# Kernel optimization log

Hardware: AMD Instinct MI355X
Metric: run time of the kernel (lower is better)

The kernel has to match this reference:

```python
import jax, jax.numpy as jnp
import numpy as np

P = 16            # num_patches = 224 // 14
T = P * P         # patches per image (256)
K = 5             # top-k templates
SIM_THR = 0.05
PATCH_THR = 2.0


def _idx2loc(idx):
    # flat patch index -> (w, h) float location, matching convert_index2location
    return jnp.stack([(idx % P).astype(jnp.float32), (idx // P).astype(jnp.float32)], axis=-1)


def setup_inputs() -> dict:
    key = jax.random.key(0)
    k1, k2, k3, k4 = jax.random.split(key, 4)
    B, N, C = 8, 32, 768
    src_feats = jax.random.normal(k1, (B, N, C, P, P), dtype=jnp.float32)
    tar_feat = jax.random.normal(k2, (B, C, P, P), dtype=jnp.float32)
    src_masks = (jax.random.uniform(k3, (B, N, P, P)) > 0.3).astype(jnp.float32)
    tar_mask = (jax.random.uniform(k4, (B, P, P)) > 0.3).astype(jnp.float32)
    return {"src_feats": src_feats, "tar_feat": tar_feat,
            "src_masks": src_masks, "tar_mask": tar_mask}


def reference(src_feats, tar_feat, src_masks, tar_mask):
    B, N, C = src_feats.shape[:3]
    # masks are already at feature resolution -> interpolate is identity; flatten
    tarm = tar_mask.reshape(B, T)                                   # (B, T)
    srcm = src_masks.reshape(B, N, T)                               # (B, N, T)
    # L2-normalize features over channel dim (F.normalize)
    tf = tar_feat / jnp.clip(jnp.linalg.norm(tar_feat, axis=1, keepdims=True), 1e-12)
    tf = tf.reshape(B, C, T)                                        # (B, C, T)
    sf = src_feats / jnp.clip(jnp.linalg.norm(src_feats, axis=2, keepdims=True), 1e-12)
    sf = sf.reshape(B, N, C, T)                                     # (B, N, C, S)
    # dense cosine similarity, masked, then thresholded to 0
    sim = jnp.einsum('bct,bncs->bnts', tf, sf)                      # (B, N, T, S)
    sim = sim * srcm[:, :, None, :] * tarm[:, None, :, None]
    sim = jnp.where(sim < SIM_THR, 0.0, sim)
    # dual nearest-neighbor search ('tar2src' direction)
    score_t2s = sim.max(axis=3)                                     # (B, N, T)
    idx_t2s = sim.argmax(axis=3).astype(jnp.int32)
    score_s2t = sim.max(axis=2)                                     # (B, N, S)
    idx_s2t = sim.argmax(axis=2).astype(jnp.int32)
    mask_sim = score_t2s >= SIM_THR
    # cycle consistency: tar -> src -> tar
    idx_s2s = jnp.take_along_axis(idx_s2t, idx_t2s, axis=2)         # (B, N, T)
    dist = jnp.linalg.norm(_idx2loc(idx_s2s) - _idx2loc(jnp.arange(T))[None, None], axis=-1)
    sim_s2s = jnp.take_along_axis(score_s2t, idx_t2s, axis=2)
    mask_cycle = (dist <= PATCH_THR) & (sim_s2s >= SIM_THR)
    # non-zero / in-mask filtering
    mask_t2s = jnp.take_along_axis(srcm, idx_t2s, axis=2)           # (B, N, T)
    mask_nz = tarm[:, None, :] * mask_t2s * (idx_s2t != 0) * (idx_t2s != 0)
    mask_all = (mask_sim & mask_cycle) * mask_nz                    # (B, N, T) float
    match_counts = mask_all.sum(axis=2)                             # (B, N)
    sim_avg = jnp.where(match_counts > 0,
                        (score_t2s * mask_all).sum(axis=2) / float(T), 0.0)
    # top-k template selection
    score_src, id_src = jax.lax.top_k(sim_avg, K)                   # (B, K)
    sel = lambda a: jnp.take_along_axis(a, id_src[:, :, None], axis=1)
    pred_mask = sel(mask_all)                                       # (B, K, T)
    score_pts = sel(score_t2s)                                      # (B, K, T)
    src_loc = _idx2loc(sel(idx_t2s)).astype(jnp.int32)              # (B, K, T, 2)
    # format_prediction: -1 outside mask, (w, h) coords inside
    grid = _idx2loc(jnp.arange(T)).astype(jnp.int32)                # (T, 2)
    nz = (pred_mask != 0)[..., None]
    tar_pts = jnp.where(nz, grid[None, None], -1)                   # (B, K, T, 2)
    src_pts = jnp.where(nz, src_loc, -1)                            # (B, K, T, 2)
    return id_src, score_src, score_pts, tar_pts, src_pts, match_counts
```

## Files before the change

kernel.cpp:

```cpp
#include <hip/hip_runtime.h>

#define T_PATCH 256
#define C_DIM   768
#define NCH     48
#define N_B     8
#define N_N     32

typedef unsigned short u16;
typedef u16   u16x8  __attribute__((ext_vector_type(8)));
typedef u16   u16x4  __attribute__((ext_vector_type(4)));
typedef short s16x8  __attribute__((ext_vector_type(8)));
typedef float f32x16 __attribute__((ext_vector_type(16)));

__device__ __forceinline__ unsigned rne16(unsigned u) {
    return (u + 0x7fffu + ((u >> 16) & 1u)) >> 16;
}

__device__ __forceinline__ void split3(float x, u16& o0, u16& o1, u16& o2) {
    unsigned u0 = rne16(__float_as_uint(x));
    float f0 = __uint_as_float(u0 << 16);
    float r1 = x - f0;
    unsigned u1 = rne16(__float_as_uint(r1));
    float f1 = __uint_as_float(u1 << 16);
    float r2 = r1 - f1;
    o0 = (u16)u0; o1 = (u16)u1; o2 = (u16)(__float_as_uint(r2) >> 16);
}

__device__ __forceinline__ void gll16(const u16* g, u16* l) {
    __builtin_amdgcn_global_load_lds(
        (const __attribute__((address_space(1))) unsigned int*)g,
        (__attribute__((address_space(3))) unsigned int*)l, 16, 0, 0);
}

__global__ void tar_split_kernel(const float* __restrict__ tar,
                                 u16* __restrict__ tS0, u16* __restrict__ tS1,
                                 u16* __restrict__ tS2, float* __restrict__ partT) {
    int blk = blockIdx.x;
    int b = blk / NCH, c = blk - b * NCH;
    int tid = threadIdx.x;
    int g = tid >> 8, t = tid & 255;
    const float* tb = tar + (size_t)b * C_DIM * T_PATCH;
    float ss = 0.f;
    u16x8 v0, v1, v2;
    #pragma unroll
    for (int j = 0; j < 8; ++j) {
        float x = tb[(c * 16 + g * 8 + j) * T_PATCH + t];
        u16 a, bb, cc;
        split3(x, a, bb, cc);
        v0[j] = a; v1[j] = bb; v2[j] = cc;
        ss = fmaf(x, x, ss);
    }
    size_t off = ((size_t)blk * 512 + tid) * 8;
    *(u16x8*)(tS0 + off) = v0;
    *(u16x8*)(tS1 + off) = v1;
    *(u16x8*)(tS2 + off) = v2;
    __shared__ float sq[512];
    sq[tid] = ss;
    __syncthreads();
    if (tid < 256) partT[blk * 256 + tid] = sq[tid] + sq[tid + 256];
}

__global__ void invt_kernel(const float* __restrict__ partT,
                            const float* __restrict__ tar_mask,
                            float* __restrict__ w_invT) {
    int b = blockIdx.x, t = threadIdx.x;
    float s = 0.f;
    for (int c = 0; c < NCH; ++c) s += partT[(b * NCH + c) * 256 + t];
    float tm = tar_mask[b * 256 + t];
    w_invT[b * 256 + t] = (tm != 0.f) ? 1.f / fmaxf(sqrtf(s), 1e-12f) : 0.f;
}

__launch_bounds__(512, 4)
__global__ void sim_kernel(const float* __restrict__ src_feats,
                           const u16* __restrict__ tS0, const u16* __restrict__ tS1,
                           const u16* __restrict__ tS2,
                           const float* __restrict__ w_invT,
                           const float* __restrict__ src_masks,
                           float* __restrict__ w_rowv, int* __restrict__ w_rowi,
                           float* __restrict__ w_s2tv, int* __restrict__ w_s2ti) {
    __shared__ __align__(16) u16 SM[36864];
    u16* Af0 = SM;
    u16* Af1 = SM + 8192;
    u16* Af2 = SM + 16384;
    u16* Bf0 = SM + 24576;
    u16* Bf1 = SM + 28672;
    u16* Bf2 = SM + 32768;
    float* sqv  = (float*)(SM);
    float* rowv = (float*)(SM + 1024);
    int*   rowi = (int*)  (SM + 3072);
    float* colv = (float*)(SM + 5120);
    int*   coli = (int*)  (SM + 6144);
    float* invT = (float*)(SM + 7168);
    float* invS = (float*)(SM + 7680);

    int bh = blockIdx.x;
    int b    = bh & 7;
    int loc  = bh >> 3;
    int n    = loc >> 1;
    int half = loc & 1;
    int bn   = b * N_N + n;
    int lbh  = bn * 2 + half;

    int tid = threadIdx.x;
    int lane = tid & 63, w = tid >> 6;
    int wm = w >> 1, wn = w & 1;
    int h = lane >> 5, l5 = lane & 31;
    int colB = tid & 127, qB = tid >> 7;
    int gq = qB >> 1, quad = qB & 1;

    const float* psrc = src_feats + (size_t)bn * C_DIM * T_PATCH
                      + (size_t)(gq * 8 + quad * 4) * T_PATCH + half * 128 + colB;
    size_t abase = (size_t)b * NCH * 4096 + (size_t)tid * 8;
    const u16* pga0 = tS0 + abase;
    const u16* pga1 = tS1 + abase;
    const u16* pga2 = tS2 + abase;

    f32x16 acc[2][2];
    #pragma unroll
    for (int i = 0; i < 2; ++i)
        #pragma unroll
        for (int j = 0; j < 2; ++j) acc[i][j] = (f32x16)0.0f;

    float sss = 0.f;

    {
        float yv[4];
        #pragma unroll
        for (int j = 0; j < 4; ++j) yv[j] = psrc[j * T_PATCH];
        psrc += 4096;
        gll16(pga0, Af0 + tid * 8);
        gll16(pga1, Af1 + tid * 8);
        gll16(pga2, Af2 + tid * 8);
        pga0 += 4096; pga1 += 4096; pga2 += 4096;
        u16x4 b0v, b1v, b2v;
        #pragma unroll
        for (int j = 0; j < 4; ++j) {
            u16 a, bb, cc;
            split3(yv[j], a, bb, cc);
            b0v[j] = a; b1v[j] = bb; b2v[j] = cc;
            sss = fmaf(yv[j], yv[j], sss);
        }
        int bslot = (gq * 128 + colB) * 8 + quad * 4;
        *(u16x4*)(Bf0 + bslot) = b0v;
        *(u16x4*)(Bf1 + bslot) = b1v;
        *(u16x4*)(Bf2 + bslot) = b2v;
    }
    __syncthreads();

    for (int c = 0; c < NCH; ++c) {
        int p = c & 1;
        bool pf = (c < NCH - 1);

        float yv[4];
        if (pf) {
            #pragma unroll
            for (int j = 0; j < 4; ++j) yv[j] = psrc[j * T_PATCH];
            psrc += 4096;
        }
        if (pf) {
            int adst = (p ^ 1) * 4096 + tid * 8;
            gll16(pga0, Af0 + adst);
            gll16(pga1, Af1 + adst);
            gll16(pga2, Af2 + adst);
            pga0 += 4096; pga1 += 4096; pga2 += 4096;
        }

        __builtin_amdgcn_s_setprio(1);
        s16x8 a0[2], a1[2], a2[2];
        {
            const u16* Ab = Af0 + p * 4096 + (h * 256 + wm * 64 + l5) * 8;
            #pragma unroll
            for (int i = 0; i < 2; ++i) a0[i] = *(const s16x8*)(Ab + i * 256);
            Ab = Af1 + p * 4096 + (h * 256 + wm * 64 + l5) * 8;
            #pragma unroll
            for (int i = 0; i < 2; ++i) a1[i] = *(const s16x8*)(Ab + i * 256);
            Ab = Af2 + p * 4096 + (h * 256 + wm * 64 + l5) * 8;
            #pragma unroll
            for (int i = 0; i < 2; ++i) a2[i] = *(const s16x8*)(Ab + i * 256);
        }
        #pragma unroll
        for (int j = 0; j < 2; ++j) {
            int boff = p * 2048 + (h * 128 + wn * 64 + j * 32 + l5) * 8;
            s16x8 b0 = *(const s16x8*)(Bf0 + boff);
            s16x8 b1 = *(const s16x8*)(Bf1 + boff);
            s16x8 b2 = *(const s16x8*)(Bf2 + boff);
            #pragma unroll
            for (int i = 0; i < 2; ++i) {
                acc[i][j] = __builtin_amdgcn_mfma_f32_32x32x16_bf16(a0[i], b0, acc[i][j], 0, 0, 0);
                acc[i][j] = __builtin_amdgcn_mfma_f32_32x32x16_bf16(a0[i], b1, acc[i][j], 0, 0, 0);
                acc[i][j] = __builtin_amdgcn_mfma_f32_32x32x16_bf16(a1[i], b0, acc[i][j], 0, 0, 0);
                acc[i][j] = __builtin_amdgcn_mfma_f32_32x32x16_bf16(a1[i], b1, acc[i][j], 0, 0, 0);
                acc[i][j] = __builtin_amdgcn_mfma_f32_32x32x16_bf16(a0[i], b2, acc[i][j], 0, 0, 0);
                acc[i][j] = __builtin_amdgcn_mfma_f32_32x32x16_bf16(a2[i], b0, acc[i][j], 0, 0, 0);
            }
        }
        __builtin_amdgcn_s_setprio(0);

        if (pf) {
            u16x4 b0v, b1v, b2v;
            #pragma unroll
            for (int j = 0; j < 4; ++j) {
                u16 a, bb, cc;
                split3(yv[j], a, bb, cc);
                b0v[j] = a; b1v[j] = bb; b2v[j] = cc;
                sss = fmaf(yv[j], yv[j], sss);
            }
            int bslot = (p ^ 1) * 2048 + (gq * 128 + colB) * 8 + quad * 4;
            *(u16x4*)(Bf0 + bslot) = b0v;
            *(u16x4*)(Bf1 + bslot) = b1v;
            *(u16x4*)(Bf2 + bslot) = b2v;
        }
        __syncthreads();
    }

    sqv[tid] = sss;
    if (tid < 256) invT[tid] = w_invT[b * 256 + tid];
    __syncthreads();
    if (tid < 128) {
        float ns = sqrtf(sqv[tid] + sqv[tid + 128] + sqv[tid + 256] + sqv[tid + 384]);
        float smv = src_masks[bn * 256 + half * 128 + tid];
        invS[tid] = (smv != 0.f) ? 1.f / fmaxf(ns, 1e-12f) : 0.f;
    }
    __syncthreads();

    float isv[2]; int sgl[2];
    #pragma unroll
    for (int j = 0; j < 2; ++j) {
        isv[j] = invS[wn * 64 + j * 32 + l5];
        sgl[j] = half * 128 + wn * 64 + j * 32 + l5;
    }
    float cbv[2]; int cbi[2];
    #pragma unroll
    for (int j = 0; j < 2; ++j) { cbv[j] = -1.f; cbi[j] = 0; }

    #pragma unroll
    for (int i = 0; i < 2; ++i) {
        #pragma unroll
        for (int r = 0; r < 16; ++r) {
            int trow = wm * 64 + i * 32 + (r & 3) + 8 * (r >> 2) + 4 * h;
            float it = invT[trow];
            float v[2];
            #pragma unroll
            for (int j = 0; j < 2; ++j) {
                float x = acc[i][j][r] * it * isv[j];
                v[j] = (x >= 0.05f) ? x : 0.f;
            }
            float bv = -1.f; int bi = 0;
            #pragma unroll
            for (int j = 0; j < 2; ++j)
                if (v[j] > bv) { bv = v[j]; bi = sgl[j]; }
            #pragma unroll
            for (int off = 1; off < 32; off <<= 1) {
                float ov = __shfl_xor(bv, off, 64);
                int   oi = __shfl_xor(bi, off, 64);
                if (ov > bv || (ov == bv && oi < bi)) { bv = ov; bi = oi; }
            }
            if (l5 == 0) { rowv[wn * 256 + trow] = bv; rowi[wn * 256 + trow] = bi; }
            #pragma unroll
            for (int j = 0; j < 2; ++j)
                if (v[j] > cbv[j]) { cbv[j] = v[j]; cbi[j] = trow; }
        }
    }
    #pragma unroll
    for (int j = 0; j < 2; ++j) {
        float bv = cbv[j]; int bi = cbi[j];
        float ov = __shfl_xor(bv, 32, 64);
        int   oi = __shfl_xor(bi, 32, 64);
        if (ov > bv || (ov == bv && oi < bi)) { bv = ov; bi = oi; }
        if (h == 0) { colv[wm * 128 + wn * 64 + j * 32 + l5] = bv;
                      coli[wm * 128 + wn * 64 + j * 32 + l5] = bi; }
    }
    __syncthreads();
    if (tid < 256) {
        float v0 = rowv[tid];       int i0 = rowi[tid];
        float v1 = rowv[256 + tid]; int i1 = rowi[256 + tid];
        if (v1 > v0 || (v1 == v0 && i1 < i0)) { v0 = v1; i0 = i1; }
        w_rowv[lbh * 256 + tid] = v0;
        w_rowi[lbh * 256 + tid] = i0;
    }
    if (tid < 128) {
        float bv = colv[tid]; int bi = coli[tid];
        #pragma unroll
        for (int q = 1; q < 4; ++q) {
            float ov = colv[q * 128 + tid]; int oi = coli[q * 128 + tid];
            if (ov > bv || (ov == bv && oi < bi)) { bv = ov; bi = oi; }
        }
        w_s2tv[bn * 256 + half * 128 + tid] = bv;
        w_s2ti[bn * 256 + half * 128 + tid] = bi;
    }
}

__global__ void combine_kernel(const float* __restrict__ w_rowv, const int* __restrict__ w_rowi,
                               const float* __restrict__ w_s2tv, const int* __restrict__ w_s2ti,
                               const float* __restrict__ src_masks, const float* __restrict__ tar_mask,
                               float* __restrict__ w_score, float* __restrict__ w_mall,
                               float* __restrict__ w_savg, int* __restrict__ w_idx,
                               float* __restrict__ out) {
    int bn = blockIdx.x; int b = bn >> 5; int t = threadIdx.x;
    __shared__ float sc_s2t[256]; __shared__ int ix_s2t[256];
    __shared__ float sm[256];
    __shared__ float red[8];
    sc_s2t[t] = w_s2tv[bn * 256 + t];
    ix_s2t[t] = w_s2ti[bn * 256 + t];
    sm[t]     = src_masks[bn * 256 + t];
    float v0 = w_rowv[(bn * 2) * 256 + t];     int i0 = w_rowi[(bn * 2) * 256 + t];
    float v1 = w_rowv[(bn * 2 + 1) * 256 + t]; int i1 = w_rowi[(bn * 2 + 1) * 256 + t];
    float st2s; int i;
    if (v1 > v0 || (v1 == v0 && i1 < i0)) { st2s = v1; i = i1; }
    else                                  { st2s = v0; i = i0; }
    float tmv = tar_mask[b * 256 + t];
    __syncthreads();

    bool msim = st2s >= 0.05f;
    int is2s = ix_s2t[i];
    int dw = (is2s & 15) - (t & 15);
    int dh = (is2s >> 4) - (t >> 4);
    bool cyc = (dw * dw + dh * dh <= 4) && (sc_s2t[i] >= 0.05f);
    float mnz = tmv * sm[i] *
                ((ix_s2t[t] != 0) ? 1.f : 0.f) *
                ((i != 0) ? 1.f : 0.f);
    float mall = (msim && cyc) ? mnz : 0.f;
    w_score[bn * 256 + t] = st2s;
    w_mall[bn * 256 + t]  = mall;
    w_idx[bn * 256 + t]   = i;

    float cnt = mall, svs = st2s * mall;
    #pragma unroll
    for (int off = 1; off < 64; off <<= 1) {
        cnt += __shfl_xor(cnt, off, 64);
        svs += __shfl_xor(svs, off, 64);
    }
    if ((t & 63) == 0) {
        red[(t >> 6) * 2]     = cnt;
        red[(t >> 6) * 2 + 1] = svs;
    }
    __syncthreads();
    if (t == 0) {
        float c = red[0] + red[2] + red[4] + red[6];
        float s = red[1] + red[3] + red[5] + red[7];
        w_savg[bn] = (c > 0.f) ? (s * (1.f / 256.f)) : 0.f;
        out[51280 + bn] = c;
    }
}

__global__ void final_kernel(const float* __restrict__ w_score,
                             const float* __restrict__ w_mall,
                             const float* __restrict__ w_savg,
                             const int*   __restrict__ w_idx,
                             float* __restrict__ out) {
    int b = blockIdx.x, tid = threadIdx.x;
    __shared__ float savg[32];
    __shared__ int   topid[5];
    __shared__ float topv[5];
    if (tid < 32) savg[tid] = w_savg[b * 32 + tid];
    __syncthreads();
    if (tid == 0) {
        unsigned used = 0;
        for (int k = 0; k < 5; ++k) {
            float bv = -1e30f; int bi = 0;
            for (int n = 0; n < 32; ++n) {
                if (!((used >> n) & 1u) && savg[n] > bv) { bv = savg[n]; bi = n; }
            }
            used |= (1u << bi);
            topid[k] = bi; topv[k] = bv;
        }
    }
    __syncthreads();
    if (tid < 5) {
        out[b * 5 + tid]      = (float)topid[tid];
        out[40 + b * 5 + tid] = topv[tid];
    }
    int t = tid;
    for (int k = 0; k < 5; ++k) {
        int bn = b * 32 + topid[k];
        float sc = w_score[bn * 256 + t];
        float ma = w_mall[bn * 256 + t];
        int   ii = w_idx[bn * 256 + t];
        int o = (b * 5 + k) * 256 + t;
        out[80 + o] = sc;
        bool nz = (ma != 0.f);
        out[10320 + 2 * o]     = nz ? (float)(t & 15)  : -1.f;
        out[10320 + 2 * o + 1] = nz ? (float)(t >> 4)  : -1.f;
        out[30800 + 2 * o]     = nz ? (float)(ii & 15) : -1.f;
        out[30800 + 2 * o + 1] = nz ? (float)(ii >> 4) : -1.f;
    }
}

extern "C" void kernel_launch(void* const* d_in, const int* in_sizes, int n_in,
                              void* d_out, int out_size, void* d_ws, size_t ws_size,
                              hipStream_t stream) {
    const float* src_feats = (const float*)d_in[0];
    const float* tar_feat  = (const float*)d_in[1];
    const float* src_masks = (const float*)d_in[2];
    const float* tar_mask  = (const float*)d_in[3];
    float* out = (float*)d_out;

    const size_t PLANE = (size_t)N_B * NCH * 512 * 8;
    u16* tS0 = (u16*)d_ws;
    u16* tS1 = tS0 + PLANE;
    u16* tS2 = tS1 + PLANE;
    float* partT  = (float*)(tS2 + PLANE);
    float* w_invT = partT + (size_t)N_B * NCH * 256;
    float* w_rowv = w_invT + 2048;
    int*   w_rowi = (int*)(w_rowv + 512 * 256);
    float* w_s2tv = (float*)(w_rowi + 512 * 256);
    int*   w_s2ti = (int*)(w_s2tv + 256 * 256);
    float* w_score = (float*)(w_s2ti + 256 * 256);
    float* w_mall  = w_score + 256 * 256;
    float* w_savg  = w_mall + 256 * 256;
    int*   w_idx   = (int*)(w_savg + 256);

    tar_split_kernel<<<N_B * NCH, 512, 0, stream>>>(tar_feat, tS0, tS1, tS2, partT);
    invt_kernel<<<N_B, 256, 0, stream>>>(partT, tar_mask, w_invT);
    sim_kernel<<<N_B * N_N * 2, 512, 0, stream>>>(src_feats, tS0, tS1, tS2, w_invT,
                                                  src_masks,
                                                  w_rowv, w_rowi, w_s2tv, w_s2ti);
    combine_kernel<<<N_B * N_N, 256, 0, stream>>>(w_rowv, w_rowi, w_s2tv, w_s2ti,
                                                  src_masks, tar_mask,
                                                  w_score, w_mall, w_savg, w_idx, out);
    final_kernel<<<N_B, 256, 0, stream>>>(w_score, w_mall, w_savg, w_idx, out);
}
```

Baseline: 372.6 us.

## Split sim kernel into quarter-column 256-thread blocks with single-buffered LDS

Each sim block now handles 64 source patches with 256 threads (4 waves) instead of 128 with 512, doubling the grid to 1024 blocks. LDS drops from double-buffered to single-buffered, with an extra barrier before the next chunk is loaded and source features prefetched two chunks ahead in registers. Row maxima are written straight to global memory per quarter, and combine_kernel merges four partials instead of two. The aim is higher occupancy and more blocks in flight, but each block now reloads the full target tile, which doubles target-side traffic, and the added barrier serializes loads against MFMA work.

```diff
diff --git a/kernel.cpp b/kernel.cpp
--- a/kernel.cpp
+++ b/kernel.cpp
@@ -70,7 +70,7 @@
     w_invT[b * 256 + t] = (tm != 0.f) ? 1.f / fmaxf(sqrtf(s), 1e-12f) : 0.f;
 }
 
-__launch_bounds__(512, 4)
+__launch_bounds__(256, 4)
 __global__ void sim_kernel(const float* __restrict__ src_feats,
                            const u16* __restrict__ tS0, const u16* __restrict__ tS1,
                            const u16* __restrict__ tS2,
@@ -78,39 +78,36 @@
                            const float* __restrict__ src_masks,
                            float* __restrict__ w_rowv, int* __restrict__ w_rowi,
                            float* __restrict__ w_s2tv, int* __restrict__ w_s2ti) {
-    __shared__ __align__(16) u16 SM[36864];
+    __shared__ __align__(16) u16 SM[15360];
     u16* Af0 = SM;
-    u16* Af1 = SM + 8192;
-    u16* Af2 = SM + 16384;
-    u16* Bf0 = SM + 24576;
-    u16* Bf1 = SM + 28672;
-    u16* Bf2 = SM + 32768;
-    float* sqv  = (float*)(SM);
-    float* rowv = (float*)(SM + 1024);
-    int*   rowi = (int*)  (SM + 3072);
-    float* colv = (float*)(SM + 5120);
-    int*   coli = (int*)  (SM + 6144);
-    float* invT = (float*)(SM + 7168);
-    float* invS = (float*)(SM + 7680);
+    u16* Af1 = SM + 4096;
+    u16* Af2 = SM + 8192;
+    u16* Bf0 = SM + 12288;
+    u16* Bf1 = SM + 13312;
+    u16* Bf2 = SM + 14336;
+    float* sqS  = (float*)(SM);
+    float* invT = (float*)(SM + 512);
+    float* invS = (float*)(SM + 1024);
+    float* colv = (float*)(SM + 1152);
+    int*   coli = (int*)  (SM + 1664);
 
     int bh = blockIdx.x;
     int b    = bh & 7;
     int loc  = bh >> 3;
-    int n    = loc >> 1;
-    int half = loc & 1;
+    int n    = loc >> 2;
+    int sq_q = loc & 3;
     int bn   = b * N_N + n;
-    int lbh  = bn * 2 + half;
+    int lbh  = bn * 4 + sq_q;
 
     int tid = threadIdx.x;
-    int lane = tid & 63, w = tid >> 6;
-    int wm = w >> 1, wn = w & 1;
+    int lane = tid & 63, wm = tid >> 6;
     int h = lane >> 5, l5 = lane & 31;
-    int colB = tid & 127, qB = tid >> 7;
+    int colB = tid & 63, qB = tid >> 6;
     int gq = qB >> 1, quad = qB & 1;
 
     const float* psrc = src_feats + (size_t)bn * C_DIM * T_PATCH
-                      + (size_t)(gq * 8 + quad * 4) * T_PATCH + half * 128 + colB;
-    size_t abase = (size_t)b * NCH * 4096 + (size_t)tid * 8;
+                      + (size_t)(qB * 4) * T_PATCH + sq_q * 64 + colB;
+    size_t abase = (size_t)b * NCH * 4096;
     const u16* pga0 = tS0 + abase;
     const u16* pga1 = tS1 + abase;
     const u16* pga2 = tS2 + abase;
@@ -123,14 +120,17 @@
 
     float sss = 0.f;
 
+    float yv[4], yv2[4];
     {
-        float yv[4];
         #pragma unroll
         for (int j = 0; j < 4; ++j) yv[j] = psrc[j * T_PATCH];
         psrc += 4096;
-        gll16(pga0, Af0 + tid * 8);
-        gll16(pga1, Af1 + tid * 8);
-        gll16(pga2, Af2 + tid * 8);
+        gll16(pga0 + tid * 8, Af0 + tid * 8);
+        gll16(pga0 + 2048 + tid * 8, Af0 + 2048 + tid * 8);
+        gll16(pga1 + tid * 8, Af1 + tid * 8);
+        gll16(pga1 + 2048 + tid * 8, Af1 + 2048 + tid * 8);
+        gll16(pga2 + tid * 8, Af2 + tid * 8);
+        gll16(pga2 + 2048 + tid * 8, Af2 + 2048 + tid * 8);
         pga0 += 4096; pga1 += 4096; pga2 += 4096;
         u16x4 b0v, b1v, b2v;
         #pragma unroll
@@ -140,47 +140,39 @@
             b0v[j] = a; b1v[j] = bb; b2v[j] = cc;
             sss = fmaf(yv[j], yv[j], sss);
         }
-        int bslot = (gq * 128 + colB) * 8 + quad * 4;
+        int bslot = (gq * 64 + colB) * 8 + quad * 4;
         *(u16x4*)(Bf0 + bslot) = b0v;
         *(u16x4*)(Bf1 + bslot) = b1v;
         *(u16x4*)(Bf2 + bslot) = b2v;
+        #pragma unroll
+        for (int j = 0; j < 4; ++j) yv[j] = psrc[j * T_PATCH];
+        psrc += 4096;
     }
     __syncthreads();
 
     for (int c = 0; c < NCH; ++c) {
-        int p = c & 1;
-        bool pf = (c < NCH - 1);
-
-        float yv[4];
-        if (pf) {
-            #pragma unroll
-            for (int j = 0; j < 4; ++j) yv[j] = psrc[j * T_PATCH];
+        if (c < NCH - 2) {
+            #pragma unroll
+            for (int j = 0; j < 4; ++j) yv2[j] = psrc[j * T_PATCH];
             psrc += 4096;
         }
-        if (pf) {
-            int adst = (p ^ 1) * 4096 + tid * 8;
-            gll16(pga0, Af0 + adst);
-            gll16(pga1, Af1 + adst);
-            gll16(pga2, Af2 + adst);
-            pga0 += 4096; pga1 += 4096; pga2 += 4096;
-        }
-
-        __builtin_amdgcn_s_setprio(1);
+
         s16x8 a0[2], a1[2], a2[2];
         {
-            const u16* Ab = Af0 + p * 4096 + (h * 256 + wm * 64 + l5) * 8;
-            #pragma unroll
-            for (int i = 0; i < 2; ++i) a0[i] = *(const s16x8*)(Ab + i * 256);
-            Ab = Af1 + p * 4096 + (h * 256 + wm * 64 + l5) * 8;
-            #pragma unroll
-            for (int i = 0; i < 2; ++i) a1[i] = *(const s16x8*)(Ab + i * 256);
-            Ab = Af2 + p * 4096 + (h * 256 + wm * 64 + l5) * 8;
-            #pragma unroll
-            for (int i = 0; i < 2; ++i) a2[i] = *(const s16x8*)(Ab + i * 256);
-        }
+            const u16* Ab0 = Af0 + (h * 256 + wm * 64 + l5) * 8;
+            const u16* Ab1 = Af1 + (h * 256 + wm * 64 + l5) * 8;
+            const u16* Ab2 = Af2 + (h * 256 + wm * 64 + l5) * 8;
+            #pragma unroll
+            for (int i = 0; i < 2; ++i) {
+                a0[i] = *(const s16x8*)(Ab0 + i * 256);
+                a1[i] = *(const s16x8*)(Ab1 + i * 256);
+                a2[i] = *(const s16x8*)(Ab2 + i * 256);
+            }
+        }
+        __builtin_amdgcn_s_setprio(1);
         #pragma unroll
         for (int j = 0; j < 2; ++j) {
-            int boff = p * 2048 + (h * 128 + wn * 64 + j * 32 + l5) * 8;
+            int boff = (h * 64 + j * 32 + l5) * 8;
             s16x8 b0 = *(const s16x8*)(Bf0 + boff);
             s16x8 b1 = *(const s16x8*)(Bf1 + boff);
             s16x8 b2 = *(const s16x8*)(Bf2 + boff);
@@ -196,7 +188,15 @@
         }
         __builtin_amdgcn_s_setprio(0);
 
-        if (pf) {
+        if (c < NCH - 1) {
+            __syncthreads();
+            gll16(pga0 + tid * 8, Af0 + tid * 8);
+            gll16(pga0 + 2048 + tid * 8, Af0 + 2048 + tid * 8);
+            gll16(pga1 + tid * 8, Af1 + tid * 8);
+            gll16(pga1 + 2048 + tid * 8, Af1 + 2048 + tid * 8);
+            gll16(pga2 + tid * 8, Af2 + tid * 8);
+            gll16(pga2 + 2048 + tid * 8, Af2 + 2048 + tid * 8);
+            pga0 += 4096; pga1 += 4096; pga2 += 4096;
             u16x4 b0v, b1v, b2v;
             #pragma unroll
             for (int j = 0; j < 4; ++j) {
@@ -205,20 +205,23 @@
                 b0v[j] = a; b1v[j] = bb; b2v[j] = cc;
                 sss = fmaf(yv[j], yv[j], sss);
             }
-            int bslot = (p ^ 1) * 2048 + (gq * 128 + colB) * 8 + quad * 4;
+            int bslot = (gq * 64 + colB) * 8 + quad * 4;
             *(u16x4*)(Bf0 + bslot) = b0v;
             *(u16x4*)(Bf1 + bslot) = b1v;
             *(u16x4*)(Bf2 + bslot) = b2v;
-        }
-        __syncthreads();
-    }
-
-    sqv[tid] = sss;
-    if (tid < 256) invT[tid] = w_invT[b * 256 + tid];
-    __syncthreads();
-    if (tid < 128) {
-        float ns = sqrtf(sqv[tid] + sqv[tid + 128] + sqv[tid + 256] + sqv[tid + 384]);
-        float smv = src_masks[bn * 256 + half * 128 + tid];
+            #pragma unroll
+            for (int j = 0; j < 4; ++j) yv[j] = yv2[j];
+            __syncthreads();
+        }
+    }
+
+    __syncthreads();
+    sqS[tid]  = sss;
+    invT[tid] = w_invT[b * 256 + tid];
+    __syncthreads();
+    if (tid < 64) {
+        float ns = sqrtf(sqS[tid] + sqS[64 + tid] + sqS[128 + tid] + sqS[192 + tid]);
+        float smv = src_masks[bn * 256 + sq_q * 64 + tid];
         invS[tid] = (smv != 0.f) ? 1.f / fmaxf(ns, 1e-12f) : 0.f;
     }
     __syncthreads();
@@ -226,8 +229,8 @@
     float isv[2]; int sgl[2];
     #pragma unroll
     for (int j = 0; j < 2; ++j) {
-        isv[j] = invS[wn * 64 + j * 32 + l5];
-        sgl[j] = half * 128 + wn * 64 + j * 32 + l5;
+        isv[j] = invS[j * 32 + l5];
+        sgl[j] = sq_q * 64 + j * 32 + l5;
     }
     float cbv[2]; int cbi[2];
     #pragma unroll
@@ -255,7 +258,10 @@
                 int   oi = __shfl_xor(bi, off, 64);
                 if (ov > bv || (ov == bv && oi < bi)) { bv = ov; bi = oi; }
             }
-            if (l5 == 0) { rowv[wn * 256 + trow] = bv; rowi[wn * 256 + trow] = bi; }
+            if (l5 == 0) {
+                w_rowv[lbh * 256 + trow] = bv;
+                w_rowi[lbh * 256 + trow] = bi;
+            }
             #pragma unroll
             for (int j = 0; j < 2; ++j)
                 if (v[j] > cbv[j]) { cbv[j] = v[j]; cbi[j] = trow; }
@@ -267,26 +273,19 @@
         float ov = __shfl_xor(bv, 32, 64);
         int   oi = __shfl_xor(bi, 32, 64);
         if (ov > bv || (ov == bv && oi < bi)) { bv = ov; bi = oi; }
-        if (h == 0) { colv[wm * 128 + wn * 64 + j * 32 + l5] = bv;
-                      coli[wm * 128 + wn * 64 + j * 32 + l5] = bi; }
-    }
-    __syncthreads();
-    if (tid < 256) {
-        float v0 = rowv[tid];       int i0 = rowi[tid];
-        float v1 = rowv[256 + tid]; int i1 = rowi[256 + tid];
-        if (v1 > v0 || (v1 == v0 && i1 < i0)) { v0 = v1; i0 = i1; }
-        w_rowv[lbh * 256 + tid] = v0;
-        w_rowi[lbh * 256 + tid] = i0;
-    }
-    if (tid < 128) {
+        if (h == 0) { colv[wm * 64 + j * 32 + l5] = bv;
+                      coli[wm * 64 + j * 32 + l5] = bi; }
+    }
+    __syncthreads();
+    if (tid < 64) {
         float bv = colv[tid]; int bi = coli[tid];
         #pragma unroll
-        for (int q = 1; q < 4; ++q) {
-            float ov = colv[q * 128 + tid]; int oi = coli[q * 128 + tid];
+        for (int m = 1; m < 4; ++m) {
+            float ov = colv[m * 64 + tid]; int oi = coli[m * 64 + tid];
             if (ov > bv || (ov == bv && oi < bi)) { bv = ov; bi = oi; }
         }
-        w_s2tv[bn * 256 + half * 128 + tid] = bv;
-        w_s2ti[bn * 256 + half * 128 + tid] = bi;
+        w_s2tv[bn * 256 + sq_q * 64 + tid] = bv;
+        w_s2ti[bn * 256 + sq_q * 64 + tid] = bi;
     }
 }
 
@@ -303,11 +302,14 @@
     sc_s2t[t] = w_s2tv[bn * 256 + t];
     ix_s2t[t] = w_s2ti[bn * 256 + t];
     sm[t]     = src_masks[bn * 256 + t];
-    float v0 = w_rowv[(bn * 2) * 256 + t];     int i0 = w_rowi[(bn * 2) * 256 + t];
-    float v1 = w_rowv[(bn * 2 + 1) * 256 + t]; int i1 = w_rowi[(bn * 2 + 1) * 256 + t];
-    float st2s; int i;
-    if (v1 > v0 || (v1 == v0 && i1 < i0)) { st2s = v1; i = i1; }
-    else                                  { st2s = v0; i = i0; }
+    float st2s = w_rowv[(bn * 4) * 256 + t];
+    int   i    = w_rowi[(bn * 4) * 256 + t];
+    #pragma unroll
+    for (int qq = 1; qq < 4; ++qq) {
+        float vq = w_rowv[(bn * 4 + qq) * 256 + t];
+        int   iq = w_rowi[(bn * 4 + qq) * 256 + t];
+        if (vq > st2s || (vq == st2s && iq < i)) { st2s = vq; i = iq; }
+    }
     float tmv = tar_mask[b * 256 + t];
     __syncthreads();
 
@@ -402,8 +404,8 @@
     float* partT  = (float*)(tS2 + PLANE);
     float* w_invT = partT + (size_t)N_B * NCH * 256;
     float* w_rowv = w_invT + 2048;
-    int*   w_rowi = (int*)(w_rowv + 512 * 256);
-    float* w_s2tv = (float*)(w_rowi + 512 * 256);
+    int*   w_rowi = (int*)(w_rowv + 1024 * 256);
+    float* w_s2tv = (float*)(w_rowi + 1024 * 256);
     int*   w_s2ti = (int*)(w_s2tv + 256 * 256);
     float* w_score = (float*)(w_s2ti + 256 * 256);
     float* w_mall  = w_score + 256 * 256;
@@ -412,7 +414,7 @@
 
     tar_split_kernel<<<N_B * NCH, 512, 0, stream>>>(tar_feat, tS0, tS1, tS2, partT);
     invt_kernel<<<N_B, 256, 0, stream>>>(partT, tar_mask, w_invT);
-    sim_kernel<<<N_B * N_N * 2, 512, 0, stream>>>(src_feats, tS0, tS1, tS2, w_invT,
+    sim_kernel<<<N_B * N_N * 4, 256, 0, stream>>>(src_feats, tS0, tS1, tS2, w_invT,
                                                   src_masks,
                                                   w_rowv, w_rowi, w_s2tv, w_s2ti);
     combine_kernel<<<N_B * N_N, 256, 0, stream>>>(w_rowv, w_rowi, w_s2tv, w_s2ti,
```

Measured after the change: 393.3 us. +5.5%, slower.

## Fuse invT into sim kernel and merge combine/final into one kernel

Applied to the files above, without the earlier changes.

Removes the separate invT kernel by having each sim block sum the target partial norms itself, and fuses combine and final into a single 8-block kernel of 1024 threads. The fused kernel recomputes the masks for the selected top-k templates instead of storing per-template scores, masks and indices to workspace. This cuts kernel launches and intermediate global traffic. In exchange, every sim block redoes a 48-step reduction over partT, and combine now runs on only 8 blocks instead of 256, so it has less parallelism.

```diff
diff --git a/kernel.cpp b/kernel.cpp
--- a/kernel.cpp
+++ b/kernel.cpp
@@ -60,21 +60,12 @@
     if (tid < 256) partT[blk * 256 + tid] = sq[tid] + sq[tid + 256];
 }
 
-__global__ void invt_kernel(const float* __restrict__ partT,
-                            const float* __restrict__ tar_mask,
-                            float* __restrict__ w_invT) {
-    int b = blockIdx.x, t = threadIdx.x;
-    float s = 0.f;
-    for (int c = 0; c < NCH; ++c) s += partT[(b * NCH + c) * 256 + t];
-    float tm = tar_mask[b * 256 + t];
-    w_invT[b * 256 + t] = (tm != 0.f) ? 1.f / fmaxf(sqrtf(s), 1e-12f) : 0.f;
-}
-
 __launch_bounds__(512, 4)
 __global__ void sim_kernel(const float* __restrict__ src_feats,
                            const u16* __restrict__ tS0, const u16* __restrict__ tS1,
                            const u16* __restrict__ tS2,
-                           const float* __restrict__ w_invT,
+                           const float* __restrict__ partT,
+                           const float* __restrict__ tar_mask,
                            const float* __restrict__ src_masks,
                            float* __restrict__ w_rowv, int* __restrict__ w_rowi,
                            float* __restrict__ w_s2tv, int* __restrict__ w_s2ti) {
@@ -214,7 +205,12 @@
     }
 
     sqv[tid] = sss;
-    if (tid < 256) invT[tid] = w_invT[b * 256 + tid];
+    if (tid < 256) {
+        float s = 0.f;
+        for (int c = 0; c < NCH; ++c) s += partT[(b * NCH + c) * 256 + tid];
+        float tm = tar_mask[b * 256 + tid];
+        invT[tid] = (tm != 0.f) ? 1.f / fmaxf(sqrtf(s), 1e-12f) : 0.f;
+    }
     __syncthreads();
     if (tid < 128) {
         float ns = sqrtf(sqv[tid] + sqv[tid + 128] + sqv[tid + 256] + sqv[tid + 384]);
@@ -290,70 +286,72 @@
     }
 }
 
-__global__ void combine_kernel(const float* __restrict__ w_rowv, const int* __restrict__ w_rowi,
-                               const float* __restrict__ w_s2tv, const int* __restrict__ w_s2ti,
-                               const float* __restrict__ src_masks, const float* __restrict__ tar_mask,
-                               float* __restrict__ w_score, float* __restrict__ w_mall,
-                               float* __restrict__ w_savg, int* __restrict__ w_idx,
-                               float* __restrict__ out) {
-    int bn = blockIdx.x; int b = bn >> 5; int t = threadIdx.x;
-    __shared__ float sc_s2t[256]; __shared__ int ix_s2t[256];
-    __shared__ float sm[256];
-    __shared__ float red[8];
-    sc_s2t[t] = w_s2tv[bn * 256 + t];
-    ix_s2t[t] = w_s2ti[bn * 256 + t];
-    sm[t]     = src_masks[bn * 256 + t];
-    float v0 = w_rowv[(bn * 2) * 256 + t];     int i0 = w_rowi[(bn * 2) * 256 + t];
-    float v1 = w_rowv[(bn * 2 + 1) * 256 + t]; int i1 = w_rowi[(bn * 2 + 1) * 256 + t];
-    float st2s; int i;
-    if (v1 > v0 || (v1 == v0 && i1 < i0)) { st2s = v1; i = i1; }
-    else                                  { st2s = v0; i = i0; }
-    float tmv = tar_mask[b * 256 + t];
-    __syncthreads();
-
-    bool msim = st2s >= 0.05f;
-    int is2s = ix_s2t[i];
-    int dw = (is2s & 15) - (t & 15);
-    int dh = (is2s >> 4) - (t >> 4);
-    bool cyc = (dw * dw + dh * dh <= 4) && (sc_s2t[i] >= 0.05f);
-    float mnz = tmv * sm[i] *
-                ((ix_s2t[t] != 0) ? 1.f : 0.f) *
-                ((i != 0) ? 1.f : 0.f);
-    float mall = (msim && cyc) ? mnz : 0.f;
-    w_score[bn * 256 + t] = st2s;
-    w_mall[bn * 256 + t]  = mall;
-    w_idx[bn * 256 + t]   = i;
-
-    float cnt = mall, svs = st2s * mall;
-    #pragma unroll
-    for (int off = 1; off < 64; off <<= 1) {
-        cnt += __shfl_xor(cnt, off, 64);
-        svs += __shfl_xor(svs, off, 64);
-    }
-    if ((t & 63) == 0) {
-        red[(t >> 6) * 2]     = cnt;
-        red[(t >> 6) * 2 + 1] = svs;
-    }
-    __syncthreads();
-    if (t == 0) {
-        float c = red[0] + red[2] + red[4] + red[6];
-        float s = red[1] + red[3] + red[5] + red[7];
-        w_savg[bn] = (c > 0.f) ? (s * (1.f / 256.f)) : 0.f;
-        out[51280 + bn] = c;
-    }
-}
-
-__global__ void final_kernel(const float* __restrict__ w_score,
-                             const float* __restrict__ w_mall,
-                             const float* __restrict__ w_savg,
-                             const int*   __restrict__ w_idx,
-                             float* __restrict__ out) {
-    int b = blockIdx.x, tid = threadIdx.x;
+__launch_bounds__(1024)
+__global__ void combine_final_kernel(const float* __restrict__ w_rowv,
+                                     const int* __restrict__ w_rowi,
+                                     const float* __restrict__ w_s2tv,
+                                     const int* __restrict__ w_s2ti,
+                                     const float* __restrict__ src_masks,
+                                     const float* __restrict__ tar_mask,
+                                     float* __restrict__ out) {
+    int b   = blockIdx.x;
+    int tid = threadIdx.x;
+    int sub = tid >> 8;
+    int t   = tid & 255;
+
+    __shared__ float sc_s2t[4][256];
+    __shared__ int   ix_s2t[4][256];
+    __shared__ float sm[4][256];
+    __shared__ float red[4][8];
     __shared__ float savg[32];
     __shared__ int   topid[5];
     __shared__ float topv[5];
-    if (tid < 32) savg[tid] = w_savg[b * 32 + tid];
-    __syncthreads();
+
+    float tmv = tar_mask[b * 256 + t];
+
+    for (int it = 0; it < 8; ++it) {
+        int bnl = it * 4 + sub;
+        int bn  = b * 32 + bnl;
+        sc_s2t[sub][t] = w_s2tv[bn * 256 + t];
+        ix_s2t[sub][t] = w_s2ti[bn * 256 + t];
+        sm[sub][t]     = src_masks[bn * 256 + t];
+        float v0 = w_rowv[(bn * 2) * 256 + t];     int i0 = w_rowi[(bn * 2) * 256 + t];
+        float v1 = w_rowv[(bn * 2 + 1) * 256 + t]; int i1 = w_rowi[(bn * 2 + 1) * 256 + t];
+        float st2s; int i;
+        if (v1 > v0 || (v1 == v0 && i1 < i0)) { st2s = v1; i = i1; }
+        else                                  { st2s = v0; i = i0; }
+        __syncthreads();
+
+        bool msim = st2s >= 0.05f;
+        int is2s = ix_s2t[sub][i];
+        int dw = (is2s & 15) - (t & 15);
+        int dh = (is2s >> 4) - (t >> 4);
+        bool cyc = (dw * dw + dh * dh <= 4) && (sc_s2t[sub][i] >= 0.05f);
+        float mnz = tmv * sm[sub][i] *
+                    ((ix_s2t[sub][t] != 0) ? 1.f : 0.f) *
+                    ((i != 0) ? 1.f : 0.f);
+        float mall = (msim && cyc) ? mnz : 0.f;
+
+        float cnt = mall, svs = st2s * mall;
+        #pragma unroll
+        for (int off = 1; off < 64; off <<= 1) {
+            cnt += __shfl_xor(cnt, off, 64);
+            svs += __shfl_xor(svs, off, 64);
+        }
+        if ((t & 63) == 0) {
+            red[sub][(t >> 6) * 2]     = cnt;
+            red[sub][(t >> 6) * 2 + 1] = svs;
+        }
+        __syncthreads();
+        if (t == 0) {
+            float c = red[sub][0] + red[sub][2] + red[sub][4] + red[sub][6];
+            float s = red[sub][1] + red[sub][3] + red[sub][5] + red[sub][7];
+            savg[bnl] = (c > 0.f) ? (s * (1.f / 256.f)) : 0.f;
+            out[51280 + bn] = c;
+        }
+        __syncthreads();
+    }
+
     if (tid == 0) {
         unsigned used = 0;
         for (int k = 0; k < 5; ++k) {
@@ -370,19 +368,43 @@
         out[b * 5 + tid]      = (float)topid[tid];
         out[40 + b * 5 + tid] = topv[tid];
     }
-    int t = tid;
-    for (int k = 0; k < 5; ++k) {
-        int bn = b * 32 + topid[k];
-        float sc = w_score[bn * 256 + t];
-        float ma = w_mall[bn * 256 + t];
-        int   ii = w_idx[bn * 256 + t];
-        int o = (b * 5 + k) * 256 + t;
-        out[80 + o] = sc;
-        bool nz = (ma != 0.f);
-        out[10320 + 2 * o]     = nz ? (float)(t & 15)  : -1.f;
-        out[10320 + 2 * o + 1] = nz ? (float)(t >> 4)  : -1.f;
-        out[30800 + 2 * o]     = nz ? (float)(ii & 15) : -1.f;
-        out[30800 + 2 * o + 1] = nz ? (float)(ii >> 4) : -1.f;
+
+    for (int kit = 0; kit < 2; ++kit) {
+        int k = kit * 4 + sub;
+        bool act = (k < 5);
+        int bnl = act ? topid[k] : 0;
+        int bn  = b * 32 + bnl;
+        float st2s = 0.f; int i = 0;
+        if (act) {
+            sc_s2t[sub][t] = w_s2tv[bn * 256 + t];
+            ix_s2t[sub][t] = w_s2ti[bn * 256 + t];
+            sm[sub][t]     = src_masks[bn * 256 + t];
+            float v0 = w_rowv[(bn * 2) * 256 + t];     int i0 = w_rowi[(bn * 2) * 256 + t];
+            float v1 = w_rowv[(bn * 2 + 1) * 256 + t]; int i1 = w_rowi[(bn * 2 + 1) * 256 + t];
+            if (v1 > v0 || (v1 == v0 && i1 < i0)) { st2s = v1; i = i1; }
+            else                                  { st2s = v0; i = i0; }
+        }
+        __syncthreads();
+        if (act) {
+            bool msim = st2s >= 0.05f;
+            int is2s = ix_s2t[sub][i];
+            int dw = (is2s & 15) - (t & 15);
+            int dh = (is2s >> 4) - (t >> 4);
+            bool cyc = (dw * dw + dh * dh <= 4) && (sc_s2t[sub][i] >= 0.05f);
+            float mnz = tmv * sm[sub][i] *
+                        ((ix_s2t[sub][t] != 0) ? 1.f : 0.f) *
+                        ((i != 0) ? 1.f : 0.f);
+            float mall = (msim && cyc) ? mnz : 0.f;
+
+            int o = (b * 5 + k) * 256 + t;
+            out[80 + o] = st2s;
+            bool nz = (mall != 0.f);
+            out[10320 + 2 * o]     = nz ? (float)(t & 15) : -1.f;
+            out[10320 + 2 * o + 1] = nz ? (float)(t >> 4) : -1.f;
+            out[30800 + 2 * o]     = nz ? (float)(i & 15) : -1.f;
+            out[30800 + 2 * o + 1] = nz ? (float)(i >> 4) : -1.f;
+        }
+        __syncthreads();
     }
 }
 
@@ -400,23 +422,15 @@
     u16* tS1 = tS0 + PLANE;
     u16* tS2 = tS1 + PLANE;
     float* partT  = (float*)(tS2 + PLANE);
-    float* w_invT = partT + (size_t)N_B * NCH * 256;
-    float* w_rowv = w_invT + 2048;
+    float* w_rowv = partT + (size_t)N_B * NCH * 256;
     int*   w_rowi = (int*)(w_rowv + 512 * 256);
     float* w_s2tv = (float*)(w_rowi + 512 * 256);
     int*   w_s2ti = (int*)(w_s2tv + 256 * 256);
-    float* w_score = (float*)(w_s2ti + 256 * 256);
-    float* w_mall  = w_score + 256 * 256;
-    float* w_savg  = w_mall + 256 * 256;
-    int*   w_idx   = (int*)(w_savg + 256);
 
     tar_split_kernel<<<N_B * NCH, 512, 0, stream>>>(tar_feat, tS0, tS1, tS2, partT);
-    invt_kernel<<<N_B, 256, 0, stream>>>(partT, tar_mask, w_invT);
-    sim_kernel<<<N_B * N_N * 2, 512, 0, stream>>>(src_feats, tS0, tS1, tS2, w_invT,
-                                                  src_masks,
+    sim_kernel<<<N_B * N_N * 2, 512, 0, stream>>>(src_feats, tS0, tS1, tS2,
+                                                  partT, tar_mask, src_masks,
                                                   w_rowv, w_rowi, w_s2tv, w_s2ti);
-    combine_kernel<<<N_B * N_N, 256, 0, stream>>>(w_rowv, w_rowi, w_s2tv, w_s2ti,
-                                                  src_masks, tar_mask,
-                                                  w_score, w_mall, w_savg, w_idx, out);
-    final_kernel<<<N_B, 256, 0, stream>>>(w_score, w_mall, w_savg, w_idx, out);
-}
+    combine_final_kernel<<<N_B, 1024, 0, stream>>>(w_rowv, w_rowi, w_s2tv, w_s2ti,
+                                                   src_masks, tar_mask, out);
+}
```

After: 376.1 us. No clear change (+0.9%).
